# Kernel tuning notes

Hardware: AMD Instinct MI355X
Metric: run time of the kernel (lower is better)

## Reference

```python
import jax, jax.numpy as jnp
import numpy as np

HEADS = 8
WS = 8  # window size


def conv1x1(x, w, b):
    # x: [B,C,H,W], w: [Cout,Cin], b: [Cout]
    return jnp.einsum('bchw,oc->bohw', x, w) + b[None, :, None, None]


def to_windows(x, heads, ws):
    # x: [B,C,H,W] -> [B*nH*nW, heads, ws*ws, C//heads]
    B, C, H, W = x.shape
    d = C // heads
    x = x.reshape(B, heads, d, H // ws, ws, W // ws, ws)
    x = x.transpose(0, 3, 5, 1, 4, 6, 2)  # B, nH, nW, heads, ws, ws, d
    return x.reshape(B * (H // ws) * (W // ws), heads, ws * ws, d)


def from_windows(xw, B, C, H, W, heads, ws):
    d = C // heads
    x = xw.reshape(B, H // ws, W // ws, heads, ws, ws, d)
    x = x.transpose(0, 3, 6, 1, 4, 2, 5)  # B, heads, d, nH, ws, nW, ws
    return x.reshape(B, C, H, W)


def setup_inputs() -> dict:
    key = jax.random.key(0)
    ks = jax.random.split(key, 10)
    B, C, H, W = 4, 256, 256, 256
    s = 0.02
    return {
        'q_feat': jax.random.normal(ks[0], (B, C, H, W), jnp.float32),
        'kv_feat': jax.random.normal(ks[1], (B, C, H, W), jnp.float32),
        'wq': jax.random.normal(ks[2], (C, C), jnp.float32) * s,
        'bq': jnp.zeros((C,), jnp.float32),
        'wk': jax.random.normal(ks[3], (C, C), jnp.float32) * s,
        'bk': jnp.zeros((C,), jnp.float32),
        'wv': jax.random.normal(ks[4], (C, C), jnp.float32) * s,
        'bv': jnp.zeros((C,), jnp.float32),
        'wp': jax.random.normal(ks[5], (C, C), jnp.float32) * s,
        'bp': jnp.zeros((C,), jnp.float32),
    }


def reference(q_feat, kv_feat, wq, bq, wk, bk, wv, bv, wp, bp):
    B, C, H, W = q_feat.shape
    heads, ws = HEADS, WS
    scale = (C // heads) ** (-0.5)

    q = to_windows(conv1x1(q_feat, wq, bq), heads, ws)   # [Nw, h, ws*ws, d]
    k = to_windows(conv1x1(kv_feat, wk, bk), heads, ws)
    v = to_windows(conv1x1(kv_feat, wv, bv), heads, ws)

    attn = jnp.einsum('whqd,whkd->whqk', q, k) * scale
    attn = jax.nn.softmax(attn, axis=-1)
    out_w = jnp.einsum('whqk,whkd->whqd', attn, v)

    out = from_windows(out_w, B, C, H, W, heads, ws)
    return conv1x1(out, wp, bp)
```

## Files before the change

### kernel.cpp

```cpp
#include <hip/hip_runtime.h>
#include <cstdint>
#include <cstddef>


typedef __attribute__((ext_vector_type(8))) short bfx8;
typedef __attribute__((ext_vector_type(4))) float f32x4;

#define HW 65536
#define NC 256
#define QKV_STRIDE 16777216UL

__device__ __forceinline__ unsigned short f2bf(float f) {
  union { float f; unsigned u; } v; v.f = f;
  unsigned r = v.u + 0x7FFFu + ((v.u >> 16) & 1u);
  return (unsigned short)(r >> 16);
}

__global__ __launch_bounds__(256) void prep_weights(
    const float* __restrict__ wq, const float* __restrict__ wk,
    const float* __restrict__ wv, const float* __restrict__ wp,
    unsigned short* __restrict__ dst) {
  int i = blockIdx.x * 256 + threadIdx.x;
  dst[i]          = f2bf(wq[i]);
  dst[i + 65536]  = f2bf(wk[i]);
  dst[i + 131072] = f2bf(wv[i]);
  int e = i & 7, lane = (i >> 3) & 63, ks = (i >> 9) & 7, ot = i >> 12;
  int src = (ot * 16 + (lane & 15)) * 256 + ks * 32 + (lane >> 4) * 8 + e;
  dst[i + 196608] = f2bf(wp[src]);
}

__device__ __forceinline__ void stage_x512(
    const float* __restrict__ x, int n0, int tid, unsigned char* __restrict__ smem) {
  const int sn = tid & 63;
  const int oc = tid >> 6;
#pragma unroll
  for (int it = 0; it < 4; ++it) {
    int c8 = (it * 8 + oc) * 8;
    const float* xp = x + (size_t)c8 * HW + n0 + sn;
    float v0 = xp[0],      v1 = xp[HW],     v2 = xp[2 * HW], v3 = xp[3 * HW];
    float v4 = xp[4 * HW], v5 = xp[5 * HW], v6 = xp[6 * HW], v7 = xp[7 * HW];
    uint4 u;
    u.x = (unsigned)f2bf(v0) | ((unsigned)f2bf(v1) << 16);
    u.y = (unsigned)f2bf(v2) | ((unsigned)f2bf(v3) << 16);
    u.z = (unsigned)f2bf(v4) | ((unsigned)f2bf(v5) << 16);
    u.w = (unsigned)f2bf(v6) | ((unsigned)f2bf(v7) << 16);
    unsigned byte = ((unsigned)(sn * 512 + c8 * 2)) ^ (((unsigned)(sn & 7)) << 4);
    *(uint4*)(smem + byte) = u;
  }
}

__device__ __forceinline__ void gemm_pass512(
    const unsigned short* __restrict__ wmat, const unsigned char* __restrict__ smem,
    int ow, int g, int qh, f32x4 (&acc)[2][4]) {
#pragma unroll
  for (int i = 0; i < 2; ++i)
#pragma unroll
    for (int j = 0; j < 4; ++j) acc[i][j] = (f32x4){0.f, 0.f, 0.f, 0.f};

  bfx8 afr[2];
#pragma unroll
  for (int mt = 0; mt < 2; ++mt)
    afr[mt] = *(const bfx8*)(wmat + (ow * 32 + mt * 16 + qh) * 256 + g * 8);

  for (int ks = 0; ks < 8; ++ks) {
    bfx8 naf[2];
    if (ks < 7) {
#pragma unroll
      for (int mt = 0; mt < 2; ++mt)
        naf[mt] = *(const bfx8*)(wmat + (ow * 32 + mt * 16 + qh) * 256 + (ks + 1) * 32 + g * 8);
    }
#pragma unroll
    for (int nt = 0; nt < 4; ++nt) {
      unsigned byte = ((unsigned)((nt * 16 + qh) * 512 + ks * 64 + g * 16)) ^
                      (((unsigned)(qh & 7)) << 4);
      bfx8 bfr = *(const bfx8*)(smem + byte);
#pragma unroll
      for (int mt = 0; mt < 2; ++mt)
        acc[mt][nt] = __builtin_amdgcn_mfma_f32_16x16x32_bf16(afr[mt], bfr, acc[mt][nt], 0, 0, 0);
    }
    if (ks < 7) { afr[0] = naf[0]; afr[1] = naf[1]; }
  }
}

__device__ __forceinline__ void store_qk512(
    const f32x4 (&acc)[2][4], const float* __restrict__ bias,
    unsigned short* __restrict__ outw, int n0, int ow, int g, int qh) {
  const int h_img = n0 >> 8, w0b = n0 & 255;
#pragma unroll
  for (int mt = 0; mt < 2; ++mt) {
    int o = ow * 32 + mt * 16 + g * 4;
    f32x4 bb = *(const f32x4*)&bias[o];
    int head = o >> 5, dbase = o & 31;
#pragma unroll
    for (int nt = 0; nt < 4; ++nt) {
      int n = nt * 16 + qh;
      int w_img = w0b + n;
      int win = ((h_img >> 3) << 5) + (w_img >> 3);
      int pos = ((h_img & 7) << 3) + (w_img & 7);
      f32x4 a = acc[mt][nt];
      uint2 pv;
      pv.x = (unsigned)f2bf(a.x + bb.x) | ((unsigned)f2bf(a.y + bb.y) << 16);
      pv.y = (unsigned)f2bf(a.z + bb.z) | ((unsigned)f2bf(a.w + bb.w) << 16);
      *(uint2*)&outw[((size_t)(win * 8 + head) * 64 + pos) * 32 + dbase] = pv;
    }
  }
}

__global__ __launch_bounds__(512) void qkv_gemm(
    const float* __restrict__ xq, const float* __restrict__ xkv,
    const unsigned short* __restrict__ wbf,
    const float* __restrict__ bq, const float* __restrict__ bk,
    const float* __restrict__ bv,
    unsigned short* __restrict__ q_w, unsigned short* __restrict__ k_w,
    unsigned short* __restrict__ v_w, int batch0, int batched) {
  __shared__ __align__(16) unsigned char bufQ[32768];
  __shared__ __align__(16) unsigned char bufKV[32768];

  const int tid = threadIdx.x;
  const int lane = tid & 63;
  const int wid = tid >> 6;
  const int g = lane >> 4;
  const int qh = lane & 15;
  const int n0 = (int)blockIdx.x * 64;
  const int batch = batch0 + blockIdx.z;
  const size_t qofs = batched ? (size_t)blockIdx.z * QKV_STRIDE : 0;
  const float* xq_b = xq + (size_t)batch * NC * HW;
  const float* xkv_b = xkv + (size_t)batch * NC * HW;

  stage_x512(xq_b, n0, tid, bufQ);
  stage_x512(xkv_b, n0, tid, bufKV);
  __syncthreads();

  f32x4 acc[2][4];
  gemm_pass512(wbf, bufQ, wid, g, qh, acc);
  store_qk512(acc, bq, q_w + qofs, n0, wid, g, qh);
  gemm_pass512(wbf + 65536, bufKV, wid, g, qh, acc);
  store_qk512(acc, bk, k_w + qofs, n0, wid, g, qh);
  gemm_pass512(wbf + 131072, bufKV, wid, g, qh, acc);

  __syncthreads();
#pragma unroll
  for (int mt = 0; mt < 2; ++mt) {
    int o = wid * 32 + mt * 16 + g * 4;
    f32x4 bb = *(const f32x4*)&bv[o];
#pragma unroll
    for (int nt = 0; nt < 4; ++nt) {
      int n = nt * 16 + qh;
      f32x4 a = acc[mt][nt];
      float vj[4] = {a.x + bb.x, a.y + bb.y, a.z + bb.z, a.w + bb.w};
#pragma unroll
      for (int j = 0; j < 4; ++j) {
        unsigned oo = (unsigned)(o + j);
        unsigned byte = (oo * 128 + (unsigned)n * 2) ^ (((oo >> 2) & 7u) << 4);
        *(unsigned short*)(bufQ + byte) = f2bf(vj[j]);
      }
    }
  }
  __syncthreads();
  const int h_img = n0 >> 8, w0b = n0 & 255;
  const int h7 = h_img & 7;
  unsigned short* vw = v_w + qofs;
#pragma unroll
  for (int it = 0; it < 4; ++it) {
    int id = it * 512 + tid;
    unsigned o = (unsigned)(id >> 3);
    int oct = id & 7;
    unsigned byte = (o * 128 + (unsigned)oct * 16) ^ (((o >> 2) & 7u) << 4);
    uint4 val = *(const uint4*)(bufQ + byte);
    int head = (int)(o >> 5), dd = (int)(o & 31);
    int win = ((h_img >> 3) << 5) + (w0b >> 3) + oct;
    *(uint4*)&vw[(size_t)(win * 8 + head) * 2048 + (size_t)(h7 * 256 + dd * 8)] = val;
  }
}

__global__ __launch_bounds__(256) void attn_conv(
    const unsigned short* __restrict__ q_w, const unsigned short* __restrict__ k_w,
    const unsigned short* __restrict__ v_w, const unsigned short* __restrict__ wpT,
    const float* __restrict__ bp, float* __restrict__ out, int batch0, int batched) {
  __shared__ unsigned short P_lds[4][2048];
  __shared__ unsigned short y_t[16384];

  const int tid = threadIdx.x;
  const int lane = tid & 63;
  const int wid = tid >> 6;
  const int g = lane >> 4;
  const int qh = lane & 15;
  const int bid = blockIdx.x;
  const int winl = ((bid & 7) << 7) | (bid >> 3);
  const int batch = batch0 + blockIdx.z;
  const size_t qofs = batched ? (size_t)blockIdx.z * QKV_STRIDE : 0;
  const float scale = 0.17677669529663687f;

  char* pbase = (char*)&P_lds[wid][0];

#pragma unroll
  for (int hi = 0; hi < 2; ++hi) {
    const int head = wid + hi * 4;
    const unsigned short* qb = q_w + qofs + (size_t)(winl * 8 + head) * 2048;
    const unsigned short* kb = k_w + qofs + (size_t)(winl * 8 + head) * 2048;
    const unsigned short* vb = v_w + qofs + (size_t)(winl * 8 + head) * 2048;

    bfx8 kf[4], qf[4];
#pragma unroll
    for (int t = 0; t < 4; ++t) {
      kf[t] = *(const bfx8*)(kb + (t * 16 + qh) * 32 + g * 8);
      qf[t] = *(const bfx8*)(qb + (t * 16 + qh) * 32 + g * 8);
    }
    f32x4 zero = {0.f, 0.f, 0.f, 0.f};
    f32x4 st[4][4];
#pragma unroll
    for (int kt = 0; kt < 4; ++kt)
#pragma unroll
      for (int qt = 0; qt < 4; ++qt)
        st[kt][qt] = __builtin_amdgcn_mfma_f32_16x16x32_bf16(kf[kt], qf[qt], zero, 0, 0, 0);

    float rv[4];
#pragma unroll
    for (int qt = 0; qt < 4; ++qt) {
      float m = -1e30f;
#pragma unroll
      for (int kt = 0; kt < 4; ++kt) {
        f32x4 v = st[kt][qt];
        m = fmaxf(m, fmaxf(fmaxf(v.x, v.y), fmaxf(v.z, v.w)));
      }
      m = fmaxf(m, __shfl_xor(m, 16, 64));
      m = fmaxf(m, __shfl_xor(m, 32, 64));
      float ssum = 0.f;
#pragma unroll
      for (int kt = 0; kt < 4; ++kt) {
        f32x4 v = st[kt][qt], e;
        e.x = __expf((v.x - m) * scale);
        e.y = __expf((v.y - m) * scale);
        e.z = __expf((v.z - m) * scale);
        e.w = __expf((v.w - m) * scale);
        ssum += e.x + e.y + e.z + e.w;
        st[kt][qt] = e;
      }
      ssum += __shfl_xor(ssum, 16, 64);
      ssum += __shfl_xor(ssum, 32, 64);
      rv[qt] = 1.f / ssum;
    }

    f32x4 ot[2][4];
#pragma unroll
    for (int dt = 0; dt < 2; ++dt)
#pragma unroll
      for (int qt = 0; qt < 4; ++qt) ot[dt][qt] = zero;

#pragma unroll
    for (int s = 0; s < 2; ++s) {
#pragma unroll
      for (int qt = 0; qt < 4; ++qt) {
        int q = qt * 16 + qh;
        unsigned sw = ((unsigned)(q & 3)) << 4;
        float r = rv[qt];
#pragma unroll
        for (int k2 = 0; k2 < 2; ++k2) {
          f32x4 e = st[s * 2 + k2][qt];
          uint2 pv;
          pv.x = (unsigned)f2bf(e.x * r) | ((unsigned)f2bf(e.y * r) << 16);
          pv.y = (unsigned)f2bf(e.z * r) | ((unsigned)f2bf(e.w * r) << 16);
          unsigned byte = ((unsigned)q * 64 + (unsigned)(k2 * 32 + g * 8)) ^ sw;
          *(uint2*)(pbase + byte) = pv;
        }
      }
      bfx8 pf[4];
#pragma unroll
      for (int qt = 0; qt < 4; ++qt) {
        int q = qt * 16 + qh;
        unsigned byte = ((unsigned)q * 64 + (unsigned)(g * 16)) ^ (((unsigned)(q & 3)) << 4);
        pf[qt] = *(const bfx8*)(pbase + byte);
      }
#pragma unroll
      for (int dt = 0; dt < 2; ++dt) {
        bfx8 vf = *(const bfx8*)(vb + (s * 4 + g) * 256 + (dt * 16 + qh) * 8);
#pragma unroll
        for (int qt = 0; qt < 4; ++qt)
          ot[dt][qt] = __builtin_amdgcn_mfma_f32_16x16x32_bf16(vf, pf[qt], ot[dt][qt], 0, 0, 0);
      }
    }

#pragma unroll
    for (int dt = 0; dt < 2; ++dt) {
      int cb = head * 32 + dt * 16 + g * 4;
#pragma unroll
      for (int qt = 0; qt < 4; ++qt) {
        int pos = qt * 16 + qh;
        f32x4 a = ot[dt][qt];
        uint2 pv;
        pv.x = (unsigned)f2bf(a.x) | ((unsigned)f2bf(a.y) << 16);
        pv.y = (unsigned)f2bf(a.z) | ((unsigned)f2bf(a.w) << 16);
        unsigned byte = ((unsigned)pos * 512 + (unsigned)cb * 2) ^ (((unsigned)(pos & 7)) << 4);
        *(uint2*)((char*)y_t + byte) = pv;
      }
    }
  }
  __syncthreads();

  f32x4 acc[4][4];
#pragma unroll
  for (int i = 0; i < 4; ++i)
#pragma unroll
    for (int j = 0; j < 4; ++j) acc[i][j] = (f32x4){0.f, 0.f, 0.f, 0.f};

  for (int ks = 0; ks < 8; ++ks) {
    bfx8 af[4];
#pragma unroll
    for (int mt = 0; mt < 4; ++mt)
      af[mt] = *(const bfx8*)(wpT + (((wid * 4 + mt) * 8 + ks) * 64 + lane) * 8);
#pragma unroll
    for (int nt = 0; nt < 4; ++nt) {
      int pos = nt * 16 + qh;
      unsigned byte = ((unsigned)pos * 512 + (unsigned)(ks * 64 + g * 16)) ^ (((unsigned)(pos & 7)) << 4);
      bfx8 bfr = *(const bfx8*)((char*)y_t + byte);
#pragma unroll
      for (int mt = 0; mt < 4; ++mt)
        acc[mt][nt] = __builtin_amdgcn_mfma_f32_16x16x32_bf16(af[mt], bfr, acc[mt][nt], 0, 0, 0);
    }
  }

  const int wrow = winl >> 5, wcol = winl & 31;
  float* ob_ = out + (size_t)batch * NC * HW;
#pragma unroll
  for (int mt = 0; mt < 4; ++mt) {
    int o0 = wid * 64 + mt * 16 + g * 4;
    float b0 = bp[o0], b1 = bp[o0 + 1], b2 = bp[o0 + 2], b3 = bp[o0 + 3];
#pragma unroll
    for (int nt = 0; nt < 4; ++nt) {
      int pos = nt * 16 + qh;
      int h_img = wrow * 8 + (pos >> 3);
      int w_img = wcol * 8 + (pos & 7);
      float* pp = ob_ + (size_t)o0 * HW + h_img * 256 + w_img;
      pp[0]      = acc[mt][nt].x + b0;
      pp[HW]     = acc[mt][nt].y + b1;
      pp[2 * HW] = acc[mt][nt].z + b2;
      pp[3 * HW] = acc[mt][nt].w + b3;
    }
  }
}

extern "C" void kernel_launch(void* const* d_in, const int* in_sizes, int n_in,
                              void* d_out, int out_size, void* d_ws, size_t ws_size,
                              hipStream_t stream) {
  const float* q_feat = (const float*)d_in[0];
  const float* kv_feat = (const float*)d_in[1];
  const float* wq = (const float*)d_in[2];
  const float* bq = (const float*)d_in[3];
  const float* wk = (const float*)d_in[4];
  const float* bk = (const float*)d_in[5];
  const float* wv = (const float*)d_in[6];
  const float* bv = (const float*)d_in[7];
  const float* wp = (const float*)d_in[8];
  const float* bp = (const float*)d_in[9];
  float* out = (float*)d_out;

  unsigned short* wbf = (unsigned short*)d_ws;
  const size_t need_batched = 524288ul + 12ul * QKV_STRIDE * 2ul;

  hipLaunchKernelGGL(prep_weights, dim3(256), dim3(256), 0, stream, wq, wk, wv, wp, wbf);

  if (ws_size >= need_batched) {
    unsigned short* q_w = wbf + 262144;
    unsigned short* k_w = q_w + 4 * QKV_STRIDE;
    unsigned short* v_w = k_w + 4 * QKV_STRIDE;
    hipLaunchKernelGGL(qkv_gemm, dim3(1024, 1, 4), dim3(512), 0, stream,
                       q_feat, kv_feat, wbf, bq, bk, bv, q_w, k_w, v_w, 0, 1);
    hipLaunchKernelGGL(attn_conv, dim3(1024, 1, 4), dim3(256), 0, stream,
                       q_w, k_w, v_w, wbf + 196608, bp, out, 0, 1);
  } else {
    unsigned short* q_w = wbf + 262144;
    unsigned short* k_w = q_w + QKV_STRIDE;
    unsigned short* v_w = k_w + QKV_STRIDE;
    for (int b = 0; b < 4; ++b) {
      hipLaunchKernelGGL(qkv_gemm, dim3(1024, 1, 1), dim3(512), 0, stream,
                         q_feat, kv_feat, wbf, bq, bk, bv, q_w, k_w, v_w, b, 0);
      hipLaunchKernelGGL(attn_conv, dim3(1024, 1, 1), dim3(256), 0, stream,
                         q_w, k_w, v_w, wbf + 196608, bp, out, b, 0);
    }
  }
}
```

Baseline: 535.5 us.

## Make QKV GEMM blocks loop over a full image row and prefetch the next tile

Each qkv_gemm block now handles one full 256-pixel image row as four 64-pixel tiles instead of a single tile, and the grid shrinks to a quarter of its former size. Global loads for the next tile's KV and Q inputs are issued into registers while the current tile's GEMMs run and V is written out. The loaded values are then packed into LDS after barriers. This aims to hide global-load latency. In exchange it uses 32 extra float registers per thread, which may lower occupancy, and with fewer blocks the GPU has less parallelism to cover stalls.

```diff
diff --git a/kernel.cpp b/kernel.cpp
--- a/kernel.cpp
+++ b/kernel.cpp
@@ -29,26 +29,6 @@
   dst[i + 196608] = f2bf(wp[src]);
 }
 
-__device__ __forceinline__ void stage_x512(
-    const float* __restrict__ x, int n0, int tid, unsigned char* __restrict__ smem) {
-  const int sn = tid & 63;
-  const int oc = tid >> 6;
-#pragma unroll
-  for (int it = 0; it < 4; ++it) {
-    int c8 = (it * 8 + oc) * 8;
-    const float* xp = x + (size_t)c8 * HW + n0 + sn;
-    float v0 = xp[0],      v1 = xp[HW],     v2 = xp[2 * HW], v3 = xp[3 * HW];
-    float v4 = xp[4 * HW], v5 = xp[5 * HW], v6 = xp[6 * HW], v7 = xp[7 * HW];
-    uint4 u;
-    u.x = (unsigned)f2bf(v0) | ((unsigned)f2bf(v1) << 16);
-    u.y = (unsigned)f2bf(v2) | ((unsigned)f2bf(v3) << 16);
-    u.z = (unsigned)f2bf(v4) | ((unsigned)f2bf(v5) << 16);
-    u.w = (unsigned)f2bf(v6) | ((unsigned)f2bf(v7) << 16);
-    unsigned byte = ((unsigned)(sn * 512 + c8 * 2)) ^ (((unsigned)(sn & 7)) << 4);
-    *(uint4*)(smem + byte) = u;
-  }
-}
-
 __device__ __forceinline__ void gemm_pass512(
     const unsigned short* __restrict__ wmat, const unsigned char* __restrict__ smem,
     int ow, int g, int qh, f32x4 (&acc)[2][4]) {
@@ -121,55 +101,98 @@
   const int wid = tid >> 6;
   const int g = lane >> 4;
   const int qh = lane & 15;
-  const int n0 = (int)blockIdx.x * 64;
+  const int row = (int)blockIdx.x;
   const int batch = batch0 + blockIdx.z;
   const size_t qofs = batched ? (size_t)blockIdx.z * QKV_STRIDE : 0;
   const float* xq_b = xq + (size_t)batch * NC * HW;
   const float* xkv_b = xkv + (size_t)batch * NC * HW;
 
-  stage_x512(xq_b, n0, tid, bufQ);
-  stage_x512(xkv_b, n0, tid, bufKV);
-  __syncthreads();
-
-  f32x4 acc[2][4];
-  gemm_pass512(wbf, bufQ, wid, g, qh, acc);
-  store_qk512(acc, bq, q_w + qofs, n0, wid, g, qh);
-  gemm_pass512(wbf + 65536, bufKV, wid, g, qh, acc);
-  store_qk512(acc, bk, k_w + qofs, n0, wid, g, qh);
-  gemm_pass512(wbf + 131072, bufKV, wid, g, qh, acc);
-
-  __syncthreads();
-#pragma unroll
-  for (int mt = 0; mt < 2; ++mt) {
-    int o = wid * 32 + mt * 16 + g * 4;
-    f32x4 bb = *(const f32x4*)&bv[o];
-#pragma unroll
-    for (int nt = 0; nt < 4; ++nt) {
-      int n = nt * 16 + qh;
-      f32x4 a = acc[mt][nt];
-      float vj[4] = {a.x + bb.x, a.y + bb.y, a.z + bb.z, a.w + bb.w};
-#pragma unroll
-      for (int j = 0; j < 4; ++j) {
-        unsigned oo = (unsigned)(o + j);
-        unsigned byte = (oo * 128 + (unsigned)n * 2) ^ (((oo >> 2) & 7u) << 4);
-        *(unsigned short*)(bufQ + byte) = f2bf(vj[j]);
-      }
-    }
-  }
-  __syncthreads();
-  const int h_img = n0 >> 8, w0b = n0 & 255;
-  const int h7 = h_img & 7;
-  unsigned short* vw = v_w + qofs;
-#pragma unroll
-  for (int it = 0; it < 4; ++it) {
-    int id = it * 512 + tid;
-    unsigned o = (unsigned)(id >> 3);
-    int oct = id & 7;
-    unsigned byte = (o * 128 + (unsigned)oct * 16) ^ (((o >> 2) & 7u) << 4);
-    uint4 val = *(const uint4*)(bufQ + byte);
-    int head = (int)(o >> 5), dd = (int)(o & 31);
-    int win = ((h_img >> 3) << 5) + (w0b >> 3) + oct;
-    *(uint4*)&vw[(size_t)(win * 8 + head) * 2048 + (size_t)(h7 * 256 + dd * 8)] = val;
+  const int sn = tid & 63;
+  const int oc = tid >> 6;
+
+  float ld[32];
+  auto issue = [&](const float* x, int t) {
+    const int n0 = row * 256 + t * 64;
+#pragma unroll
+    for (int it = 0; it < 4; ++it) {
+      int c8 = (it * 8 + oc) * 8;
+      const float* xp = x + (size_t)c8 * HW + n0 + sn;
+#pragma unroll
+      for (int j = 0; j < 8; ++j) ld[it * 8 + j] = xp[(size_t)j * HW];
+    }
+  };
+  auto pack = [&](unsigned char* dst) {
+#pragma unroll
+    for (int it = 0; it < 4; ++it) {
+      int c8 = (it * 8 + oc) * 8;
+      uint4 u;
+      u.x = (unsigned)f2bf(ld[it * 8 + 0]) | ((unsigned)f2bf(ld[it * 8 + 1]) << 16);
+      u.y = (unsigned)f2bf(ld[it * 8 + 2]) | ((unsigned)f2bf(ld[it * 8 + 3]) << 16);
+      u.z = (unsigned)f2bf(ld[it * 8 + 4]) | ((unsigned)f2bf(ld[it * 8 + 5]) << 16);
+      u.w = (unsigned)f2bf(ld[it * 8 + 6]) | ((unsigned)f2bf(ld[it * 8 + 7]) << 16);
+      unsigned byte = ((unsigned)(sn * 512 + c8 * 2)) ^ (((unsigned)(sn & 7)) << 4);
+      *(uint4*)(dst + byte) = u;
+    }
+  };
+
+  issue(xq_b, 0);  pack(bufQ);
+  issue(xkv_b, 0); pack(bufKV);
+
+  for (int t = 0; t < 4; ++t) {
+    __syncthreads();
+    const int n0 = row * 256 + t * 64;
+
+    f32x4 acc[2][4];
+    gemm_pass512(wbf, bufQ, wid, g, qh, acc);
+    store_qk512(acc, bq, q_w + qofs, n0, wid, g, qh);
+    gemm_pass512(wbf + 65536, bufKV, wid, g, qh, acc);
+    store_qk512(acc, bk, k_w + qofs, n0, wid, g, qh);
+    if (t < 3) issue(xkv_b, t + 1);
+    gemm_pass512(wbf + 131072, bufKV, wid, g, qh, acc);
+
+    __syncthreads();
+
+#pragma unroll
+    for (int mt = 0; mt < 2; ++mt) {
+      int o = wid * 32 + mt * 16 + g * 4;
+      f32x4 bb = *(const f32x4*)&bv[o];
+#pragma unroll
+      for (int nt = 0; nt < 4; ++nt) {
+        int n = nt * 16 + qh;
+        f32x4 a = acc[mt][nt];
+        float vj[4] = {a.x + bb.x, a.y + bb.y, a.z + bb.z, a.w + bb.w};
+#pragma unroll
+        for (int j = 0; j < 4; ++j) {
+          unsigned oo = (unsigned)(o + j);
+          unsigned byte = (oo * 128 + (unsigned)n * 2) ^ (((oo >> 2) & 7u) << 4);
+          *(unsigned short*)(bufQ + byte) = f2bf(vj[j]);
+        }
+      }
+    }
+    if (t < 3) pack(bufKV);
+
+    __syncthreads();
+
+    {
+      const int h7 = row & 7;
+      unsigned short* vw = v_w + qofs;
+#pragma unroll
+      for (int it = 0; it < 4; ++it) {
+        int id = it * 512 + tid;
+        unsigned o = (unsigned)(id >> 3);
+        int oct = id & 7;
+        unsigned byte = (o * 128 + (unsigned)oct * 16) ^ (((o >> 2) & 7u) << 4);
+        uint4 val = *(const uint4*)(bufQ + byte);
+        int head = (int)(o >> 5), dd = (int)(o & 31);
+        int win = ((row >> 3) << 5) + t + oct;
+        win = ((row >> 3) << 5) + t * 8 + oct;
+        *(uint4*)&vw[(size_t)(win * 8 + head) * 2048 + (size_t)(h7 * 256 + dd * 8)] = val;
+      }
+    }
+    if (t < 3) issue(xq_b, t + 1);
+
+    __syncthreads();
+    if (t < 3) pack(bufQ);
   }
 }
 
@@ -363,7 +386,7 @@
     unsigned short* q_w = wbf + 262144;
     unsigned short* k_w = q_w + 4 * QKV_STRIDE;
     unsigned short* v_w = k_w + 4 * QKV_STRIDE;
-    hipLaunchKernelGGL(qkv_gemm, dim3(1024, 1, 4), dim3(512), 0, stream,
+    hipLaunchKernelGGL(qkv_gemm, dim3(256, 1, 4), dim3(512), 0, stream,
                        q_feat, kv_feat, wbf, bq, bk, bv, q_w, k_w, v_w, 0, 1);
     hipLaunchKernelGGL(attn_conv, dim3(1024, 1, 4), dim3(256), 0, stream,
                        q_w, k_w, v_w, wbf + 196608, bp, out, 0, 1);
@@ -372,7 +395,7 @@
     unsigned short* k_w = q_w + QKV_STRIDE;
     unsigned short* v_w = k_w + QKV_STRIDE;
     for (int b = 0; b < 4; ++b) {
-      hipLaunchKernelGGL(qkv_gemm, dim3(1024, 1, 1), dim3(512), 0, stream,
+      hipLaunchKernelGGL(qkv_gemm, dim3(256, 1, 1), dim3(512), 0, stream,
                          q_feat, kv_feat, wbf, bq, bk, bv, q_w, k_w, v_w, b, 0);
       hipLaunchKernelGGL(attn_conv, dim3(1024, 1, 1), dim3(256), 0, stream,
                          q_w, k_w, v_w, wbf + 196608, bp, out, b, 0);
```

New measurement: 1.327 ms. 2.48x slower.
